# Kernel tuning notes

Measured on AMD Instinct MI355X. Metric: run time of the kernel, lower is better.

The kernel has to match this reference:

```python
import jax, jax.numpy as jnp
import numpy as np

C, FF, NH = 128, 2048, 8
B, D, H, W = 1, 16, 16, 16
EPS = 1e-5

def setup_inputs() -> dict:
    key = jax.random.key(0)
    ks = jax.random.split(key, 20)
    s = 0.02
    inp = {
        'x': jax.random.normal(ks[0], (B, C, D, H, W), jnp.float32),
        'Wq': jax.random.normal(ks[1], (C, C), jnp.float32) * s,
        'bq': jnp.zeros((C,), jnp.float32),
        'Wk': jax.random.normal(ks[2], (C, C), jnp.float32) * s,
        'bk': jnp.zeros((C,), jnp.float32),
        'Wv': jax.random.normal(ks[3], (C, C), jnp.float32) * s,
        'bv': jnp.zeros((C,), jnp.float32),
        'Wo': jax.random.normal(ks[4], (C, C), jnp.float32) * s,
        'bo': jnp.zeros((C,), jnp.float32),
        'W1': jax.random.normal(ks[5], (FF, C), jnp.float32) * s,
        'b1': jnp.zeros((FF,), jnp.float32),
        'W2': jax.random.normal(ks[6], (C, FF), jnp.float32) * s,
        'b2': jnp.zeros((C,), jnp.float32),
        'g1': jnp.ones((C,), jnp.float32),
        'be1': jnp.zeros((C,), jnp.float32),
        'g2': jnp.ones((C,), jnp.float32),
        'be2': jnp.zeros((C,), jnp.float32),
    }
    return inp

def _layernorm(t, g, b):
    # normalize over last (channel) dim, biased variance like torch LayerNorm
    m = jnp.mean(t, axis=-1, keepdims=True)
    v = jnp.mean(jnp.square(t - m), axis=-1, keepdims=True)
    return (t - m) * jax.lax.rsqrt(v + EPS) * g + b

def reference(x, Wq, bq, Wk, bk, Wv, bv, Wo, bo, W1, b1, W2, b2, g1, be1, g2, be2):
    b_, c, d, h, w = x.shape
    n = d * h * w
    hd = c // NH
    xf = x.reshape(b_, c, n)  # [B,C,N]
    # 1x1 conv3d == per-voxel linear over channels
    q = jnp.einsum('oc,bcn->bon', Wq, xf) + bq[:, None]
    k = jnp.einsum('oc,bcn->bon', Wk, xf) + bk[:, None]
    v = jnp.einsum('oc,bcn->bon', Wv, xf) + bv[:, None]
    q = q.reshape(b_, NH, hd, n)
    k = k.reshape(b_, NH, hd, n)
    v = v.reshape(b_, NH, hd, n)
    scores = jnp.einsum('bhcd,bhce->bhde', q, k) / (hd ** 0.5)  # [B,NH,N,N]
    probs = jax.nn.softmax(scores, axis=-1)
    attn = jnp.einsum('bhde,bhce->bhcd', probs, v).reshape(b_, c, n)
    attn = jnp.einsum('oc,bcn->bon', Wo, attn) + bo[:, None]
    x1 = xf + attn  # residual (dropout = identity at eval)
    x1 = _layernorm(x1.transpose(0, 2, 1), g1, be1)  # [B,N,C]
    hmid = jax.nn.relu(jnp.einsum('fc,bnc->bnf', W1, x1) + b1)
    ffn = jnp.einsum('cf,bnf->bnc', W2, hmid) + b2
    x2 = _layernorm(x1 + ffn, g2, be2)
    return x2.transpose(0, 2, 1).reshape(b_, c, d, h, w)
```

## Files before the change

### kernel.cpp

```cpp
#include <hip/hip_runtime.h>
#include <hip/hip_bf16.h>

typedef __hip_bfloat16 bf16;
typedef short short8 __attribute__((ext_vector_type(8)));
typedef float f32x4 __attribute__((ext_vector_type(4)));
typedef unsigned int u32x4 __attribute__((ext_vector_type(4)));

#define C_   128
#define N_   4096
#define NH_  8
#define HD_  16
#define FF_  2048
#define SCALE_Q 0.360673760222241f

__device__ __forceinline__ unsigned short f2bf_bits(float f) {
    bf16 h = __float2bfloat16(f);
    return *reinterpret_cast<unsigned short*>(&h);
}
__device__ __forceinline__ unsigned int pack_trunc(float lo, float hi) {
    return __builtin_amdgcn_perm(__float_as_uint(hi), __float_as_uint(lo), 0x07060302u);
}
__device__ __forceinline__ short f2bf_trunc(float f) {
    return (short)(__float_as_uint(f) >> 16);
}
__device__ __forceinline__ float bfs2f(short s) {
    return __uint_as_float(((unsigned int)(unsigned short)s) << 16);
}
__device__ __forceinline__ float fast_exp2(float x) {
    return __builtin_amdgcn_exp2f(x);
}
__device__ __forceinline__ f32x4 mfma16(short8 a, short8 b, f32x4 c) {
    return __builtin_amdgcn_mfma_f32_16x16x32_bf16(a, b, c, 0, 0, 0);
}

__global__ void __launch_bounds__(256) k_prep(
    const float* __restrict__ Wq, const float* __restrict__ Wk,
    const float* __restrict__ Wv, const float* __restrict__ Wo,
    const float* __restrict__ W1, const float* __restrict__ W2,
    const float* __restrict__ x,
    bf16* __restrict__ Wqkvf, bf16* __restrict__ Wof,
    bf16* __restrict__ W1f, bf16* __restrict__ W2f,
    bf16* __restrict__ xTf)
{
    const int i = blockIdx.x * 256 + threadIdx.x;
    if (i < 73728) {
        const float* row;
        bf16* dst;
        int kblk, g;
        if (i < 8192) {
            const int o = i >> 4;
            kblk = (i >> 2) & 3; g = i & 3;
            const int odx = (o < 384) ? o : o - 384;
            row = (o < 128) ? (Wq + o * 128)
                : (o < 256) ? (Wk + (o - 128) * 128)
                : (o < 384) ? (Wv + (o - 256) * 128)
                            : (Wo + (o - 384) * 128);
            bf16* buf = (o < 384) ? Wqkvf : Wof;
            dst = buf + ((((odx >> 4) << 2) + kblk) * 512 + ((g << 4) + (odx & 15)) * 8);
        } else if (i < 40960) {
            const int t = i - 8192, o = t >> 4;
            kblk = (t >> 2) & 3; g = t & 3;
            row = W1 + o * 128;
            dst = W1f + ((((o >> 4) << 2) + kblk) * 512 + ((g << 4) + (o & 15)) * 8);
        } else {
            const int t = i - 40960, o = t >> 8;
            kblk = (t >> 2) & 63; g = t & 3;
            row = W2 + o * 2048;
            dst = W2f + ((((o >> 4) << 6) + kblk) * 512 + ((g << 4) + (o & 15)) * 8);
        }
        const int k0 = kblk * 32 + g * 4;
        const f32x4 lo = *(const f32x4*)(row + k0);
        const f32x4 hi = *(const f32x4*)(row + k0 + 16);
        u32x4 w;
        #pragma unroll
        for (int j = 0; j < 4; ++j)
            w[j] = ((unsigned int)f2bf_bits(hi[j]) << 16) | f2bf_bits(lo[j]);
        *(u32x4*)dst = w;
    } else {
        const int t = i - 73728;
        const int n = t & 4095, g = (t >> 12) & 3, cblk = t >> 14;
        const int c0 = cblk * 32 + g * 4;
        const float* xs = x + (size_t)c0 * 4096 + n;
        u32x4 w;
        #pragma unroll
        for (int j = 0; j < 4; ++j)
            w[j] = ((unsigned int)f2bf_bits(xs[(size_t)(16 + j) * 4096]) << 16)
                 | f2bf_bits(xs[(size_t)j * 4096]);
        bf16* dst = xTf + ((((n >> 4) << 2) + cblk) * 512 + ((g << 4) + (n & 15)) * 8);
        *(u32x4*)dst = w;
    }
}

__global__ void __launch_bounds__(256) k_qkv(
    const bf16* __restrict__ xTf, const bf16* __restrict__ Wqkvf,
    const float* __restrict__ bq, const float* __restrict__ bk, const float* __restrict__ bv,
    bf16* __restrict__ qf, bf16* __restrict__ kf, bf16* __restrict__ vf)
{
    const int tid = threadIdx.x, wave = tid >> 6, lane = tid & 63;
    const int col = lane & 15, quad = lane >> 4;
    const int gw = blockIdx.x * 4 + wave;
    const int rt = gw / 24, ct = gw % 24;
    f32x4 acc = {};
    #pragma unroll
    for (int c = 0; c < 4; ++c) {
        short8 a = *(const short8*)(xTf + ((size_t)(rt * 4 + c) << 9) + lane * 8);
        short8 b = *(const short8*)(Wqkvf + ((size_t)(ct * 4 + c) << 9) + lane * 8);
        acc = mfma16(a, b, acc);
    }
    #pragma unroll
    for (int r = 0; r < 4; ++r) {
        const int m = rt * 16 + quad * 4 + r;
        const int n = ct * 16 + col;
        const float v = acc[r];
        if (n < 128) {
            const int h = n >> 4, ch = n & 15;
            qf[((h << 8) + (m >> 4)) * 256 + (((ch >> 3) << 4) + (m & 15)) * 8 + (ch & 7)] =
                __float2bfloat16((v + bq[n]) * SCALE_Q);
        } else if (n < 256) {
            const int c2 = n - 128, h = c2 >> 4, ch = c2 & 15;
            kf[((h << 8) + (m >> 4)) * 256 + (((ch >> 3) << 4) + (m & 15)) * 8 + (ch & 7)] =
                __float2bfloat16(v + bk[c2]);
        } else {
            const int c2 = n - 256, h = c2 >> 4, ch = c2 & 15;
            const int ko = m & 31;
            const int pos = ((ko & 15) << 1) + (ko >> 4);
            vf[((h << 7) + (m >> 5)) * 512 + (((pos >> 3) << 4) + ch) * 8 + (pos & 7)] =
                __float2bfloat16(v + bv[c2]);
        }
    }
}

__global__ void __launch_bounds__(256)
attn_kernel(const bf16* __restrict__ qf, const bf16* __restrict__ kf,
            const bf16* __restrict__ vf, bf16* __restrict__ af)
{
    __shared__ __align__(16) union {
        unsigned int P[4][4][2][320];
        float comb[4][4][64][8];
    } sh;
    const int tid = threadIdx.x, wave = tid >> 6, lane = tid & 63;
    const int col = lane & 15, quad = lane >> 4;
    const int gw = blockIdx.x;
    const int h  = gw >> 6;
    const int tile0 = (gw & 63) << 2;
    const f32x4 zero = {};

    short8 aq[4] = {{}, {}, {}, {}};
    if (quad < 2) {
        #pragma unroll
        for (int qt = 0; qt < 4; ++qt)
            aq[qt] = *(const short8*)(qf + ((size_t)((h << 8) + tile0 + qt) << 8) + lane * 8);
    }

    const short8 onesb = { (short)0x3F80, (short)0x3F80, (short)0x3F80, (short)0x3F80,
                           (short)0x3F80, (short)0x3F80, (short)0x3F80, (short)0x3F80 };

    f32x4 accO[4] = {{}, {}, {}, {}};
    f32x4 accL[4] = {{}, {}, {}, {}};

    const int kbeg = wave << 10;

    for (int i = 0; i < 32; i += 2) {
        const int mA = kbeg + (i << 5);
        const int mB = mA + 32;

        short8 bkA0 = {}, bkA1 = {}, bkB0 = {}, bkB1 = {};
        if (quad < 2) {
            const bf16* ka = kf + ((size_t)((h << 8) + (mA >> 4)) << 8) + lane * 8;
            bkA0 = *(const short8*)(ka);
            bkA1 = *(const short8*)(ka + 256);
            bkB0 = *(const short8*)(ka + 512);
            bkB1 = *(const short8*)(ka + 768);
        }
        const short8 vA = *(const short8*)(vf + ((size_t)((h << 7) + (mA >> 5)) << 9) + lane * 8);
        const short8 vB = *(const short8*)(vf + ((size_t)((h << 7) + (mB >> 5)) << 9) + lane * 8);

        #pragma unroll
        for (int qt = 0; qt < 4; ++qt) {
            f32x4 s0 = mfma16(aq[qt], bkA0, zero);
            f32x4 s1 = mfma16(aq[qt], bkA1, zero);
            f32x4 s2 = mfma16(aq[qt], bkB0, zero);
            f32x4 s3 = mfma16(aq[qt], bkB1, zero);
            unsigned int* P0 = &sh.P[wave][qt][0][0];
            unsigned int* P1 = &sh.P[wave][qt][1][0];
            #pragma unroll
            for (int r = 0; r < 4; ++r) {
                P0[(quad * 4 + r) * 20 + col] = pack_trunc(fast_exp2(s0[r]), fast_exp2(s1[r]));
                P1[(quad * 4 + r) * 20 + col] = pack_trunc(fast_exp2(s2[r]), fast_exp2(s3[r]));
            }
        }
        #pragma unroll
        for (int qt = 0; qt < 4; ++qt) {
            const short* Ps0 = (const short*)&sh.P[wave][qt][0][0];
            const short* Ps1 = (const short*)&sh.P[wave][qt][1][0];
            short8 ap0 = *(const short8*)(Ps0 + col * 40 + quad * 8);
            accO[qt] = mfma16(ap0, vA, accO[qt]);
            accL[qt] = mfma16(ap0, onesb, accL[qt]);
            short8 ap1 = *(const short8*)(Ps1 + col * 40 + quad * 8);
            accO[qt] = mfma16(ap1, vB, accO[qt]);
            accL[qt] = mfma16(ap1, onesb, accL[qt]);
        }
    }

    __syncthreads();
    #pragma unroll
    for (int qt = 0; qt < 4; ++qt)
        #pragma unroll
        for (int r = 0; r < 4; ++r) {
            sh.comb[qt][wave][lane][r]     = accO[qt][r];
            sh.comb[qt][wave][lane][4 + r] = accL[qt][r];
        }
    __syncthreads();

    {
        const int qt = wave, tile = tile0 + qt;
        #pragma unroll
        for (int r = 0; r < 4; ++r) {
            float O = sh.comb[qt][0][lane][r] + sh.comb[qt][1][lane][r]
                    + sh.comb[qt][2][lane][r] + sh.comb[qt][3][lane][r];
            float l = sh.comb[qt][0][lane][4+r] + sh.comb[qt][1][lane][4+r]
                    + sh.comb[qt][2][lane][4+r] + sh.comb[qt][3][lane][4+r];
            const int row16 = quad * 4 + r;
            const int pk = (col << 1) + (h & 1);
            af[((tile << 2) + (h >> 1)) * 512 + (((pk >> 3) << 4) + row16) * 8 + (pk & 7)] =
                __float2bfloat16(O / l);
        }
    }
}

__global__ void __launch_bounds__(512, 2)
k_mega(const bf16* __restrict__ af, const bf16* __restrict__ xTf,
       const bf16* __restrict__ Wof, const bf16* __restrict__ W1f, const bf16* __restrict__ W2f,
       const float* __restrict__ bo, const float* __restrict__ b1, const float* __restrict__ b2,
       const float* __restrict__ g1, const float* __restrict__ be1,
       const float* __restrict__ g2, const float* __restrict__ be2,
       float* __restrict__ out)
{
    __shared__ __align__(16) unsigned int Pb[8][2][320];
    __shared__ float comb[224][64];
    const int tid = threadIdx.x, wave = tid >> 6, lane = tid & 63;
    const int col = lane & 15, quad = lane >> 4;
    const int rt = blockIdx.x, n0 = rt << 4;
    const f32x4 zero = {};

    short8 ao[4], xt[4];
    #pragma unroll
    for (int c = 0; c < 4; ++c) {
        ao[c] = *(const short8*)(af  + ((size_t)(rt * 4 + c) << 9) + lane * 8);
        xt[c] = *(const short8*)(xTf + ((size_t)(rt * 4 + c) << 9) + lane * 8);
    }
    f32x4 d[8];
    #pragma unroll
    for (int t = 0; t < 8; ++t) d[t] = zero;
    #pragma unroll
    for (int t = 0; t < 8; ++t)
        #pragma unroll
        for (int c = 0; c < 4; ++c) {
            short8 b = *(const short8*)(Wof + ((size_t)(t * 4 + c) << 9) + lane * 8);
            d[t] = mfma16(ao[c], b, d[t]);
        }
    #pragma unroll
    for (int t = 0; t < 8; ++t) {
        const float bt = bo[t * 16 + col];
        #pragma unroll
        for (int r = 0; r < 4; ++r) d[t][r] += bt;
    }

    float x1f[4][8];
    #pragma unroll
    for (int c = 0; c < 4; ++c) {
        unsigned int* Pw = &Pb[wave][c & 1][0];
        const short* Ps = (const short*)Pw;
        #pragma unroll
        for (int r = 0; r < 4; ++r)
            Pw[(quad * 4 + r) * 20 + col] = pack_trunc(d[2 * c][r], d[2 * c + 1][r]);
        short8 ar = *(const short8*)(Ps + col * 40 + quad * 8);
        #pragma unroll
        for (int j = 0; j < 8; ++j)
            x1f[c][j] = bfs2f(ar[j]) + bfs2f(xt[c][j]);
    }

    float s = 0.f, ss = 0.f;
    #pragma unroll
    for (int c = 0; c < 4; ++c)
        #pragma unroll
        for (int j = 0; j < 8; ++j) { s += x1f[c][j]; ss += x1f[c][j] * x1f[c][j]; }
    s  += __shfl_xor(s, 16);  s  += __shfl_xor(s, 32);
    ss += __shfl_xor(ss, 16); ss += __shfl_xor(ss, 32);
    const float m1 = s * (1.f / 128.f);
    const float rstd1 = rsqrtf(ss * (1.f / 128.f) - m1 * m1 + 1e-5f);
    short8 aq1[4];
    #pragma unroll
    for (int c = 0; c < 4; ++c)
        #pragma unroll
        for (int j = 0; j < 8; ++j) {
            const int pos = quad * 8 + j;
            const int ko = ((pos & 1) << 4) + (pos >> 1);
            const int ch = c * 32 + ko;
            aq1[c][j] = f2bf_trunc((x1f[c][j] - m1) * rstd1 * g1[ch] + be1[ch]);
        }

    f32x4 ACC[8];
    #pragma unroll
    for (int t = 0; t < 8; ++t) ACC[t] = zero;
    for (int i = 0; i < 8; ++i) {
        const int ffc = (wave << 3) + i;
        f32x4 p0 = zero, p1 = zero;
        #pragma unroll
        for (int c = 0; c < 4; ++c) {
            short8 b = *(const short8*)(W1f + ((size_t)(ffc * 8 + c) << 9) + lane * 8);
            p0 = mfma16(aq1[c], b, p0);
        }
        #pragma unroll
        for (int c = 0; c < 4; ++c) {
            short8 b = *(const short8*)(W1f + ((size_t)(ffc * 8 + 4 + c) << 9) + lane * 8);
            p1 = mfma16(aq1[c], b, p1);
        }
        const float bb0 = b1[ffc * 32 + col], bb1 = b1[ffc * 32 + 16 + col];
        unsigned int* Pw = &Pb[wave][i & 1][0];
        #pragma unroll
        for (int r = 0; r < 4; ++r)
            Pw[(quad * 4 + r) * 20 + col] =
                pack_trunc(fmaxf(p0[r] + bb0, 0.f), fmaxf(p1[r] + bb1, 0.f));
        short8 ah = *(const short8*)((const short*)Pw + col * 40 + quad * 8);
        #pragma unroll
        for (int t = 0; t < 8; ++t) {
            short8 bw = *(const short8*)(W2f + ((size_t)(t * 64 + ffc) << 9) + lane * 8);
            ACC[t] = mfma16(ah, bw, ACC[t]);
        }
    }

    if (wave) {
        #pragma unroll
        for (int t = 0; t < 8; ++t)
            #pragma unroll
            for (int r = 0; r < 4; ++r)
                comb[(wave - 1) * 32 + t * 4 + r][lane] = ACC[t][r];
    }
    __syncthreads();
    if (wave == 0) {
        #pragma unroll
        for (int t = 0; t < 8; ++t)
            #pragma unroll
            for (int r = 0; r < 4; ++r) {
                float acc = ACC[t][r];
                #pragma unroll
                for (int w = 0; w < 7; ++w)
                    acc += comb[w * 32 + t * 4 + r][lane];
                ACC[t][r] = acc;
            }
        short* xb = (short*)&Pb[0][0][0];
        #pragma unroll
        for (int c = 0; c < 4; ++c)
            *(short8*)(xb + (col * 4 + c) * 32 + quad * 8) = aq1[c];
        float t2[8][4];
        #pragma unroll
        for (int t = 0; t < 8; ++t) {
            const int ch = t * 16 + col;
            const int pk = (col << 1) + (t & 1);
            const int c = t >> 1;
            const float bb = b2[ch];
            #pragma unroll
            for (int r = 0; r < 4; ++r)
                t2[t][r] = ACC[t][r] + bb + bfs2f(xb[((quad * 4 + r) * 4 + c) * 32 + pk]);
        }
        #pragma unroll
        for (int r = 0; r < 4; ++r) {
            float S = 0.f, SS = 0.f;
            #pragma unroll
            for (int t = 0; t < 8; ++t) { S += t2[t][r]; SS += t2[t][r] * t2[t][r]; }
            S  += __shfl_xor(S, 1);  S  += __shfl_xor(S, 2);
            S  += __shfl_xor(S, 4);  S  += __shfl_xor(S, 8);
            SS += __shfl_xor(SS, 1); SS += __shfl_xor(SS, 2);
            SS += __shfl_xor(SS, 4); SS += __shfl_xor(SS, 8);
            const float m2 = S * (1.f / 128.f);
            const float rstd2 = rsqrtf(SS * (1.f / 128.f) - m2 * m2 + 1e-5f);
            #pragma unroll
            for (int t = 0; t < 8; ++t) {
                const int ch = t * 16 + col;
                out[(size_t)ch * N_ + n0 + quad * 4 + r] =
                    (t2[t][r] - m2) * rstd2 * g2[ch] + be2[ch];
            }
        }
    }
}

extern "C" void kernel_launch(void* const* d_in, const int* in_sizes, int n_in,
                              void* d_out, int out_size, void* d_ws, size_t ws_size,
                              hipStream_t stream) {
    const float* x   = (const float*)d_in[0];
    const float* Wq  = (const float*)d_in[1];
    const float* bq  = (const float*)d_in[2];
    const float* Wk  = (const float*)d_in[3];
    const float* bk  = (const float*)d_in[4];
    const float* Wv  = (const float*)d_in[5];
    const float* bv  = (const float*)d_in[6];
    const float* Wo  = (const float*)d_in[7];
    const float* bo  = (const float*)d_in[8];
    const float* W1  = (const float*)d_in[9];
    const float* b1  = (const float*)d_in[10];
    const float* W2  = (const float*)d_in[11];
    const float* b2  = (const float*)d_in[12];
    const float* g1  = (const float*)d_in[13];
    const float* be1 = (const float*)d_in[14];
    const float* g2  = (const float*)d_in[15];
    const float* be2 = (const float*)d_in[16];
    float* out = (float*)d_out;

    char* ws = (char*)d_ws;
    bf16* xTf   = (bf16*)(ws + 0);
    bf16* qf    = (bf16*)(ws + 1048576);
    bf16* kf    = (bf16*)(ws + 2097152);
    bf16* vf    = (bf16*)(ws + 3145728);
    bf16* af    = (bf16*)(ws + 4194304);
    bf16* Wqkvf = (bf16*)(ws + 5242880);
    bf16* Wof   = (bf16*)(ws + 5341184);
    bf16* W1f   = (bf16*)(ws + 5373952);
    bf16* W2f   = (bf16*)(ws + 5898240);

    k_prep<<<544, 256, 0, stream>>>(Wq, Wk, Wv, Wo, W1, W2, x, Wqkvf, Wof, W1f, W2f, xTf);
    k_qkv<<<1536, 256, 0, stream>>>(xTf, Wqkvf, bq, bk, bv, qf, kf, vf);
    attn_kernel<<<512, 256, 0, stream>>>(qf, kf, vf, af);
    k_mega<<<256, 512, 0, stream>>>(af, xTf, Wof, W1f, W2f, bo, b1, b2,
                                    g1, be1, g2, be2, out);
}
```

Before: 139.2 us.

## Process two row tiles per k_mega block to reuse W1/W2 fragment loads

Each k_mega block now handles two 16-row tiles instead of one and launches half as many blocks. Each wave loads its W1 and W2 fragments once and applies them to both tiles, which halves weight traffic per output row. The price is more registers (two accumulator sets), an extra LDS exchange and barrier for the normalized activations, and only 128 blocks on the device, which may leave CUs idle and lowers occupancy.

New measurement: 142.0 us. Within noise of the previous version (+2.0%).

```diff
diff --git a/kernel.cpp b/kernel.cpp
--- a/kernel.cpp
+++ b/kernel.cpp
@@ -228,7 +228,7 @@
     }
 }
 
-__global__ void __launch_bounds__(512, 2)
+__global__ void __launch_bounds__(512)
 k_mega(const bf16* __restrict__ af, const bf16* __restrict__ xTf,
        const bf16* __restrict__ Wof, const bf16* __restrict__ W1f, const bf16* __restrict__ W2f,
        const float* __restrict__ bo, const float* __restrict__ b1, const float* __restrict__ b2,
@@ -237,10 +237,12 @@
        float* __restrict__ out)
 {
     __shared__ __align__(16) unsigned int Pb[8][2][320];
-    __shared__ float comb[224][64];
+    __shared__ __align__(16) short aqs[2][4][512];
+    __shared__ float comb[7][64][64];
     const int tid = threadIdx.x, wave = tid >> 6, lane = tid & 63;
     const int col = lane & 15, quad = lane >> 4;
-    const int rt = blockIdx.x, n0 = rt << 4;
+    const int rtl = wave & 1;
+    const int rt = (blockIdx.x << 1) + rtl;
     const f32x4 zero = {};
 
     short8 ao[4], xt[4];
@@ -300,54 +302,96 @@
             aq1[c][j] = f2bf_trunc((x1f[c][j] - m1) * rstd1 * g1[ch] + be1[ch]);
         }
 
-    f32x4 ACC[8];
-    #pragma unroll
-    for (int t = 0; t < 8; ++t) ACC[t] = zero;
+    if (wave < 2) {
+        #pragma unroll
+        for (int c = 0; c < 4; ++c)
+            *(short8*)&aqs[rtl][c][lane * 8] = aq1[c];
+    }
+    __syncthreads();
+    short8 aqr0[4], aqr1[4];
+    if (rtl == 0) {
+        #pragma unroll
+        for (int c = 0; c < 4; ++c) {
+            aqr0[c] = aq1[c];
+            aqr1[c] = *(const short8*)&aqs[1][c][lane * 8];
+        }
+    } else {
+        #pragma unroll
+        for (int c = 0; c < 4; ++c) {
+            aqr1[c] = aq1[c];
+            aqr0[c] = *(const short8*)&aqs[0][c][lane * 8];
+        }
+    }
+
+    f32x4 ACC0[8], ACC1[8];
+    #pragma unroll
+    for (int t = 0; t < 8; ++t) { ACC0[t] = zero; ACC1[t] = zero; }
+    #pragma unroll 2
     for (int i = 0; i < 8; ++i) {
         const int ffc = (wave << 3) + i;
+        short8 w1r[8];
+        #pragma unroll
+        for (int c = 0; c < 8; ++c)
+            w1r[c] = *(const short8*)(W1f + ((size_t)(ffc * 8 + c) << 9) + lane * 8);
+        const float bb0 = b1[ffc * 32 + col], bb1 = b1[ffc * 32 + 16 + col];
         f32x4 p0 = zero, p1 = zero;
         #pragma unroll
-        for (int c = 0; c < 4; ++c) {
-            short8 b = *(const short8*)(W1f + ((size_t)(ffc * 8 + c) << 9) + lane * 8);
-            p0 = mfma16(aq1[c], b, p0);
-        }
-        #pragma unroll
-        for (int c = 0; c < 4; ++c) {
-            short8 b = *(const short8*)(W1f + ((size_t)(ffc * 8 + 4 + c) << 9) + lane * 8);
-            p1 = mfma16(aq1[c], b, p1);
-        }
-        const float bb0 = b1[ffc * 32 + col], bb1 = b1[ffc * 32 + 16 + col];
-        unsigned int* Pw = &Pb[wave][i & 1][0];
+        for (int c = 0; c < 4; ++c) p0 = mfma16(aqr0[c], w1r[c], p0);
+        #pragma unroll
+        for (int c = 0; c < 4; ++c) p1 = mfma16(aqr0[c], w1r[4 + c], p1);
+        unsigned int* Pw0 = &Pb[wave][0][0];
         #pragma unroll
         for (int r = 0; r < 4; ++r)
-            Pw[(quad * 4 + r) * 20 + col] =
+            Pw0[(quad * 4 + r) * 20 + col] =
                 pack_trunc(fmaxf(p0[r] + bb0, 0.f), fmaxf(p1[r] + bb1, 0.f));
-        short8 ah = *(const short8*)((const short*)Pw + col * 40 + quad * 8);
+        short8 ah0 = *(const short8*)((const short*)Pw0 + col * 40 + quad * 8);
+        f32x4 q0 = zero, q1 = zero;
+        #pragma unroll
+        for (int c = 0; c < 4; ++c) q0 = mfma16(aqr1[c], w1r[c], q0);
+        #pragma unroll
+        for (int c = 0; c < 4; ++c) q1 = mfma16(aqr1[c], w1r[4 + c], q1);
+        unsigned int* Pw1 = &Pb[wave][1][0];
+        #pragma unroll
+        for (int r = 0; r < 4; ++r)
+            Pw1[(quad * 4 + r) * 20 + col] =
+                pack_trunc(fmaxf(q0[r] + bb0, 0.f), fmaxf(q1[r] + bb1, 0.f));
+        short8 ah1 = *(const short8*)((const short*)Pw1 + col * 40 + quad * 8);
         #pragma unroll
         for (int t = 0; t < 8; ++t) {
             short8 bw = *(const short8*)(W2f + ((size_t)(t * 64 + ffc) << 9) + lane * 8);
-            ACC[t] = mfma16(ah, bw, ACC[t]);
-        }
-    }
-
-    if (wave) {
+            ACC0[t] = mfma16(ah0, bw, ACC0[t]);
+            ACC1[t] = mfma16(ah1, bw, ACC1[t]);
+        }
+    }
+
+    if (wave >= 1) {
         #pragma unroll
         for (int t = 0; t < 8; ++t)
             #pragma unroll
             for (int r = 0; r < 4; ++r)
-                comb[(wave - 1) * 32 + t * 4 + r][lane] = ACC[t][r];
+                comb[wave - 1][t * 4 + r][lane] = ACC0[t][r];
+    }
+    if (wave != 1) {
+        const int slot = (wave == 0) ? 0 : wave - 1;
+        #pragma unroll
+        for (int t = 0; t < 8; ++t)
+            #pragma unroll
+            for (int r = 0; r < 4; ++r)
+                comb[slot][32 + t * 4 + r][lane] = ACC1[t][r];
     }
     __syncthreads();
+
     if (wave == 0) {
+        const int n0 = rt << 4;
         #pragma unroll
         for (int t = 0; t < 8; ++t)
             #pragma unroll
             for (int r = 0; r < 4; ++r) {
-                float acc = ACC[t][r];
+                float a = ACC0[t][r];
                 #pragma unroll
                 for (int w = 0; w < 7; ++w)
-                    acc += comb[w * 32 + t * 4 + r][lane];
-                ACC[t][r] = acc;
+                    a += comb[w][t * 4 + r][lane];
+                ACC0[t][r] = a;
             }
         short* xb = (short*)&Pb[0][0][0];
         #pragma unroll
@@ -362,7 +406,53 @@
             const float bb = b2[ch];
             #pragma unroll
             for (int r = 0; r < 4; ++r)
-                t2[t][r] = ACC[t][r] + bb + bfs2f(xb[((quad * 4 + r) * 4 + c) * 32 + pk]);
+                t2[t][r] = ACC0[t][r] + bb + bfs2f(xb[((quad * 4 + r) * 4 + c) * 32 + pk]);
+        }
+        #pragma unroll
+        for (int r = 0; r < 4; ++r) {
+            float S = 0.f, SS = 0.f;
+            #pragma unroll
+            for (int t = 0; t < 8; ++t) { S += t2[t][r]; SS += t2[t][r] * t2[t][r]; }
+            S  += __shfl_xor(S, 1);  S  += __shfl_xor(S, 2);
+            S  += __shfl_xor(S, 4);  S  += __shfl_xor(S, 8);
+            SS += __shfl_xor(SS, 1); SS += __shfl_xor(SS, 2);
+            SS += __shfl_xor(SS, 4); SS += __shfl_xor(SS, 8);
+            const float m2 = S * (1.f / 128.f);
+            const float rstd2 = rsqrtf(SS * (1.f / 128.f) - m2 * m2 + 1e-5f);
+            #pragma unroll
+            for (int t = 0; t < 8; ++t) {
+                const int ch = t * 16 + col;
+                out[(size_t)ch * N_ + n0 + quad * 4 + r] =
+                    (t2[t][r] - m2) * rstd2 * g2[ch] + be2[ch];
+            }
+        }
+    }
+    if (wave == 1) {
+        const int n0 = rt << 4;
+        #pragma unroll
+        for (int t = 0; t < 8; ++t)
+            #pragma unroll
+            for (int r = 0; r < 4; ++r) {
+                float a = comb[0][32 + t * 4 + r][lane] + ACC1[t][r];
+                #pragma unroll
+                for (int s2 = 1; s2 < 7; ++s2)
+                    a += comb[s2][32 + t * 4 + r][lane];
+                ACC1[t][r] = a;
+            }
+        short* xb = (short*)&Pb[4][0][0];
+        #pragma unroll
+        for (int c = 0; c < 4; ++c)
+            *(short8*)(xb + (col * 4 + c) * 32 + quad * 8) = aq1[c];
+        float t2[8][4];
+        #pragma unroll
+        for (int t = 0; t < 8; ++t) {
+            const int ch = t * 16 + col;
+            const int pk = (col << 1) + (t & 1);
+            const int c = t >> 1;
+            const float bb = b2[ch];
+            #pragma unroll
+            for (int r = 0; r < 4; ++r)
+                t2[t][r] = ACC1[t][r] + bb + bfs2f(xb[((quad * 4 + r) * 4 + c) * 32 + pk]);
         }
         #pragma unroll
         for (int r = 0; r < 4; ++r) {
@@ -421,6 +511,6 @@
     k_prep<<<544, 256, 0, stream>>>(Wq, Wk, Wv, Wo, W1, W2, x, Wqkvf, Wof, W1f, W2f, xTf);
     k_qkv<<<1536, 256, 0, stream>>>(xTf, Wqkvf, bq, bk, bv, qf, kf, vf);
     attn_kernel<<<512, 256, 0, stream>>>(qf, kf, vf, af);
-    k_mega<<<256, 512, 0, stream>>>(af, xTf, Wof, W1f, W2f, bo, b1, b2,
+    k_mega<<<128, 512, 0, stream>>>(af, xTf, Wof, W1f, W2f, bo, b1, b2,
                                     g1, be1, g2, be2, out);
 }
```
